# Kernel tuning notes

Hardware: AMD Instinct MI355X
Metric: run time of the kernel (lower is better)

## Reference

```python
import jax, jax.numpy as jnp
import numpy as np

EPS = 1e-8
NUM_ITERS = 2

def _ln(x, g, b, eps=1e-6):
    mu = jnp.mean(x, axis=-1, keepdims=True)
    var = jnp.mean((x - mu) ** 2, axis=-1, keepdims=True)
    return (x - mu) * jax.lax.rsqrt(var + eps) * g + b

def setup_inputs() -> dict:
    key = jax.random.key(0)
    ks = jax.random.split(key, 16)
    B, O, L, M, S, H = 64, 11, 4096, 256, 256, 1024
    def xavier(k, shape):
        fan_in, fan_out = shape[1], shape[0]
        lim = float(np.sqrt(6.0 / (fan_in + fan_out)))
        return jax.random.uniform(k, shape, jnp.float32, -lim, lim)
    return {
        "slots": jax.random.normal(ks[0], (B, O, S), jnp.float32),
        "inputs": jax.random.normal(ks[1], (B, L, M), jnp.float32),
        "ln_in_g": jnp.ones((M,), jnp.float32),
        "ln_in_b": jnp.zeros((M,), jnp.float32),
        "Wk": xavier(ks[2], (S, M)),
        "Wv": xavier(ks[3], (S, M)),
        "ln_q_g": jnp.ones((S,), jnp.float32),
        "ln_q_b": jnp.zeros((S,), jnp.float32),
        "Wq": xavier(ks[4], (S, S)),
        "gru_wi": xavier(ks[5], (3 * S, S)),
        "gru_wh": xavier(ks[6], (3 * S, S)),
        "gru_bi": jnp.zeros((3 * S,), jnp.float32),
        "gru_bh": jnp.zeros((3 * S,), jnp.float32),
        "ln_m_g": jnp.ones((S,), jnp.float32),
        "ln_m_b": jnp.zeros((S,), jnp.float32),
        "W1": xavier(ks[7], (H, S)),
        "b1": jnp.zeros((H,), jnp.float32),
        "W2": xavier(ks[8], (S, H)),
        "b2": jnp.zeros((S,), jnp.float32),
    }

def reference(slots, inputs, ln_in_g, ln_in_b, Wk, Wv, ln_q_g, ln_q_b, Wq,
              gru_wi, gru_wh, gru_bi, gru_bh, ln_m_g, ln_m_b, W1, b1, W2, b2):
    D = slots.shape[-1]
    scale = D ** -0.5  # head_dim = qkv_size (num_heads=1)
    x = _ln(inputs, ln_in_g, ln_in_b)          # [B,L,M]
    k = x @ Wk.T                                # [B,L,S]
    v = x @ Wv.T                                # [B,L,S]
    attn = None
    for _ in range(NUM_ITERS):
        sn = _ln(slots, ln_q_g, ln_q_b)
        q = (sn @ Wq.T) * scale                 # [B,O,S]
        logits = jnp.einsum('bqd,bkd->bqk', q, k)  # [B,O,L]
        attn = jax.nn.softmax(logits, axis=-2)     # inverted: over slots (queries)
        attn_n = attn / (jnp.sum(attn, axis=-1, keepdims=True) + EPS)
        updates = jnp.einsum('bqk,bkd->bqd', attn_n, v)  # [B,O,S]
        # GRU cell update
        gi = updates @ gru_wi.T + gru_bi
        gh = slots @ gru_wh.T + gru_bh
        ir, iz, inn = jnp.split(gi, 3, axis=-1)
        hr, hz, hn = jnp.split(gh, 3, axis=-1)
        r = jax.nn.sigmoid(ir + hr)
        z = jax.nn.sigmoid(iz + hz)
        n = jnp.tanh(inn + r * hn)
        slots = (1.0 - z) * n + z * slots
        # pre-LN residual MLP
        h = _ln(slots, ln_m_g, ln_m_b)
        slots = slots + (jax.nn.relu(h @ W1.T + b1) @ W2.T + b2)
    return (slots, attn)
```

## Files before the change

kernel.cpp:

```cpp
#include <hip/hip_runtime.h>
#include <hip/hip_bf16.h>


using f32x4 = __attribute__((ext_vector_type(4))) float;
using s16x8 = __attribute__((ext_vector_type(8))) short;

#define MFMA_B16(a,b,c) __builtin_amdgcn_mfma_f32_16x16x32_bf16((a),(b),(c),0,0,0)

static __device__ __forceinline__ short f2bf(float f) {
  union { __hip_bfloat16 h; short s; } u; u.h = __float2bfloat16(f); return u.s;
}
static __device__ __forceinline__ s16x8 zero8() {
  s16x8 z;
#pragma unroll
  for (int i = 0; i < 8; i++) z[i] = 0;
  return z;
}

enum : size_t {
  OFF_WKB  = 0,
  OFF_WVB  = OFF_WKB + 131072,
  OFF_WQB  = OFF_WVB + 131072,
  OFF_WIB  = OFF_WQB + 131072,
  OFF_WHB  = OFF_WIB + 393216,
  OFF_W1B  = OFF_WHB + 393216,
  OFF_W2B  = OFF_W1B + 524288,
  OFF_QB   = OFF_W2B + 524288,
  OFF_UPDB = OFF_QB  + 360448,
  OFF_SAF  = OFF_UPDB + 360448,
  OFF_SAB  = OFF_SAF + 720896,
  OFF_SBF  = OFF_SAB + 360448,
  OFF_SBB  = OFF_SBF + 720896,
  OFF_HIDB = OFF_SBB + 360448,
  OFF_NUM  = OFF_HIDB + 1441792,
  OFF_DEN  = OFF_NUM + 720896,
  OFF_KB   = OFF_DEN + 3072,
  OFF_VB   = OFF_KB + 134217728,
  WS_NEED  = OFF_VB + 134217728
};

__global__ __launch_bounds__(256) void prep_kernel(
    const float* __restrict__ Wk, const float* __restrict__ Wv, const float* __restrict__ Wq,
    const float* __restrict__ Wi, const float* __restrict__ Wh,
    const float* __restrict__ W1, const float* __restrict__ W2,
    const float* __restrict__ slots,
    short* __restrict__ WkB, short* __restrict__ WvB, short* __restrict__ WqB,
    short* __restrict__ WiB, short* __restrict__ WhB,
    short* __restrict__ W1B, short* __restrict__ W2B,
    float* __restrict__ SaF, short* __restrict__ SaB)
{
  int idx = blockIdx.x * 256 + threadIdx.x;
  int stride = gridDim.x * 256;
  for (int i = idx; i < 256*256; i += stride) { WkB[i]=f2bf(Wk[i]); WvB[i]=f2bf(Wv[i]); WqB[i]=f2bf(Wq[i]); }
  for (int i = idx; i < 768*256; i += stride) { WiB[i]=f2bf(Wi[i]); WhB[i]=f2bf(Wh[i]); }
  for (int i = idx; i < 1024*256; i += stride) { W1B[i]=f2bf(W1[i]); W2B[i]=f2bf(W2[i]); }
  for (int i = idx; i < 704*256; i += stride) { float v = slots[i]; SaF[i]=v; SaB[i]=f2bf(v); }
}

__global__ __launch_bounds__(256) void kv_kernel(
    const float* __restrict__ inputs, const float* __restrict__ lng, const float* __restrict__ lnb,
    const short* __restrict__ WkB, const short* __restrict__ WvB,
    short* __restrict__ kB, short* __restrict__ vB)
{
  __shared__ short xt[128][264];
  const int b = blockIdx.y;
  const int l0 = blockIdx.x * 128;
  const int tid = threadIdx.x;
  const int w = tid >> 6, lane = tid & 63;
  const int grp = lane >> 4, li = lane & 15;

  float4 g4 = *(const float4*)(lng + lane*4);
  float4 b4 = *(const float4*)(lnb + lane*4);
  for (int i = 0; i < 32; i++) {
    int row = w*32 + i;
    const float4 x = *(const float4*)(inputs + ((size_t)(b*4096 + l0 + row))*256 + lane*4);
    float s = x.x+x.y+x.z+x.w;
    float ss = x.x*x.x + x.y*x.y + x.z*x.z + x.w*x.w;
#pragma unroll
    for (int m = 1; m < 64; m <<= 1) { s += __shfl_xor(s, m); ss += __shfl_xor(ss, m); }
    float mu = s * 0.00390625f;
    float rs = rsqrtf(ss*0.00390625f - mu*mu + 1e-6f);
    short4 o;
    o.x = f2bf((x.x-mu)*rs*g4.x + b4.x);
    o.y = f2bf((x.y-mu)*rs*g4.y + b4.y);
    o.z = f2bf((x.z-mu)*rs*g4.z + b4.z);
    o.w = f2bf((x.w-mu)*rs*g4.w + b4.w);
    *(short4*)(&xt[row][lane*4]) = o;
  }
  __syncthreads();

  const short* Wbase = (w < 2) ? WkB : WvB;
  const int nwave = (w & 1) * 128;
  for (int nt = 0; nt < 8; nt++) {
    const int ncol = nwave + nt*16 + li;
    s16x8 bw[8];
    const short* wp = Wbase + (size_t)ncol*256 + grp*8;
#pragma unroll
    for (int kt = 0; kt < 8; kt++) bw[kt] = *(const s16x8*)(wp + kt*32);
    for (int mp = 0; mp < 4; mp++) {
      s16x8 a0[8], a1[8];
#pragma unroll
      for (int kt = 0; kt < 8; kt++) {
        a0[kt] = *(const s16x8*)(&xt[mp*32 + li][kt*32 + grp*8]);
        a1[kt] = *(const s16x8*)(&xt[mp*32 + 16 + li][kt*32 + grp*8]);
      }
      f32x4 c0 = {0,0,0,0}, c1 = {0,0,0,0};
#pragma unroll
      for (int kt = 0; kt < 8; kt++) {
        c0 = MFMA_B16(a0[kt], bw[kt], c0);
        c1 = MFMA_B16(a1[kt], bw[kt], c1);
      }
      const int row0 = mp*32 + grp*4;
      if (w < 2) {
#pragma unroll
        for (int r = 0; r < 4; r++) {
          kB[((size_t)(b*4096 + l0 + row0 + r))*256 + ncol]      = f2bf(c0[r]);
          kB[((size_t)(b*4096 + l0 + row0 + 16 + r))*256 + ncol] = f2bf(c1[r]);
        }
      } else {
        short4 p0, p1;
        p0.x=f2bf(c0[0]); p0.y=f2bf(c0[1]); p0.z=f2bf(c0[2]); p0.w=f2bf(c0[3]);
        p1.x=f2bf(c1[0]); p1.y=f2bf(c1[1]); p1.z=f2bf(c1[2]); p1.w=f2bf(c1[3]);
        short* vp = vB + ((size_t)(b*256 + ncol))*4096 + l0 + row0;
        *(short4*)vp = p0;
        *(short4*)(vp + 16) = p1;
      }
    }
  }
}

__global__ __launch_bounds__(256) void slotpre_kernel(
    const float* __restrict__ SaF, const float* __restrict__ lng, const float* __restrict__ lnb,
    const short* __restrict__ WqB, short* __restrict__ qB,
    float* __restrict__ numF, float* __restrict__ denF)
{
  __shared__ float red0[16][16], red1[16][16];
  __shared__ float mu_s[16], rs_s[16];
  __shared__ short hl[16][264];
  const int mt = blockIdx.x, nb = blockIdx.y;
  const int tid = threadIdx.x;
  {
    int gidx = (blockIdx.y*44 + blockIdx.x)*256 + tid;
    for (int i = gidx; i < 704*256; i += 44*4*256) numF[i] = 0.0f;
    if (gidx < 704) denF[gidx] = 0.0f;
  }
  const int rr = tid & 15, cs = tid >> 4;
  const float* rp = SaF + (size_t)(mt*16 + rr)*256 + cs*16;
  float s = 0.f, ss = 0.f;
#pragma unroll
  for (int i = 0; i < 16; i++) { float x = rp[i]; s += x; ss += x*x; }
  red0[rr][cs] = s; red1[rr][cs] = ss;
  __syncthreads();
  if (tid < 16) {
    float ts = 0.f, tss = 0.f;
#pragma unroll
    for (int i = 0; i < 16; i++) { ts += red0[tid][i]; tss += red1[tid][i]; }
    float mu = ts * 0.00390625f;
    mu_s[tid] = mu; rs_s[tid] = rsqrtf(tss*0.00390625f - mu*mu + 1e-6f);
  }
  __syncthreads();
  {
    float mu = mu_s[rr], rs = rs_s[rr];
#pragma unroll
    for (int i = 0; i < 16; i++) { int c = cs*16 + i; hl[rr][c] = f2bf((rp[i]-mu)*rs*lng[c] + lnb[c]); }
  }
  __syncthreads();
  const int w = tid >> 6, lane = tid & 63, grp = lane >> 4, li = lane & 15;
  const int n = nb*64 + w*16 + li;
  f32x4 acc = {0,0,0,0};
  const short* wp = WqB + (size_t)n*256 + grp*8;
#pragma unroll
  for (int kt = 0; kt < 8; kt++)
    acc = MFMA_B16(*(const s16x8*)(&hl[li][kt*32 + grp*8]), *(const s16x8*)(wp + kt*32), acc);
#pragma unroll
  for (int r = 0; r < 4; r++)
    qB[(size_t)(mt*16 + grp*4 + r)*256 + n] = f2bf(acc[r] * 0.0625f);
}

__global__ __launch_bounds__(256) void attn_kernel(
    const short* __restrict__ qB, const short* __restrict__ kB, const short* __restrict__ vB,
    float* __restrict__ numF, float* __restrict__ denF,
    float* __restrict__ attn_out, const int write_attn)
{
  __shared__ short plds[4][16][40];
  const int b = blockIdx.y;
  const int tid = threadIdx.x;
  const int w = tid >> 6, lane = tid & 63, grp = lane >> 4, li = lane & 15;
  const int nvalid = (grp < 2) ? 4 : (grp == 2 ? 3 : 0);

  s16x8 aq[8];
  if (li < 11) {
    const short* qp = qB + (size_t)(b*11 + li)*256 + grp*8;
#pragma unroll
    for (int kt = 0; kt < 8; kt++) aq[kt] = *(const s16x8*)(qp + kt*32);
  } else {
#pragma unroll
    for (int kt = 0; kt < 8; kt++) aq[kt] = zero8();
  }
  f32x4 zf = {0,0,0,0};
  f32x4 accu[16];
#pragma unroll
  for (int st = 0; st < 16; st++) accu[st] = zf;
  float dacc[4] = {0.f, 0.f, 0.f, 0.f};

  for (int p = 0; p < 4; p++) {
    const int l0 = blockIdx.x*512 + w*128 + p*32;
    f32x4 c0 = zf, c1 = zf;
    const short* kp = kB + ((size_t)(b*4096 + l0 + li))*256 + grp*8;
#pragma unroll
    for (int kt = 0; kt < 8; kt++) c0 = MFMA_B16(aq[kt], *(const s16x8*)(kp + kt*32), c0);
#pragma unroll
    for (int kt = 0; kt < 8; kt++) c1 = MFMA_B16(aq[kt], *(const s16x8*)(kp + 16*256 + kt*32), c1);

    float a0[4], a1[4];
    {
      float mx = -1e30f;
#pragma unroll
      for (int r = 0; r < 4; r++) if (r < nvalid) mx = fmaxf(mx, c0[r]);
      mx = fmaxf(mx, __shfl_xor(mx, 16)); mx = fmaxf(mx, __shfl_xor(mx, 32));
      float sm = 0.f;
#pragma unroll
      for (int r = 0; r < 4; r++) { a0[r] = (r < nvalid) ? __expf(c0[r]-mx) : 0.f; sm += a0[r]; }
      sm += __shfl_xor(sm, 16); sm += __shfl_xor(sm, 32);
      float inv = 1.0f / sm;
#pragma unroll
      for (int r = 0; r < 4; r++) { a0[r] *= inv; dacc[r] += a0[r]; }
    }
    {
      float mx = -1e30f;
#pragma unroll
      for (int r = 0; r < 4; r++) if (r < nvalid) mx = fmaxf(mx, c1[r]);
      mx = fmaxf(mx, __shfl_xor(mx, 16)); mx = fmaxf(mx, __shfl_xor(mx, 32));
      float sm = 0.f;
#pragma unroll
      for (int r = 0; r < 4; r++) { a1[r] = (r < nvalid) ? __expf(c1[r]-mx) : 0.f; sm += a1[r]; }
      sm += __shfl_xor(sm, 16); sm += __shfl_xor(sm, 32);
      float inv = 1.0f / sm;
#pragma unroll
      for (int r = 0; r < 4; r++) { a1[r] *= inv; dacc[r] += a1[r]; }
    }
    if (write_attn) {
#pragma unroll
      for (int r = 0; r < 4; r++) if (r < nvalid) {
        attn_out[(size_t)(b*11 + grp*4 + r)*4096 + l0 + li]      = a0[r];
        attn_out[(size_t)(b*11 + grp*4 + r)*4096 + l0 + 16 + li] = a1[r];
      }
    }
#pragma unroll
    for (int r = 0; r < 4; r++) {
      plds[w][grp*4 + r][li]      = (r < nvalid) ? f2bf(a0[r]) : (short)0;
      plds[w][grp*4 + r][16 + li] = (r < nvalid) ? f2bf(a1[r]) : (short)0;
    }
    asm volatile("s_waitcnt lgkmcnt(0)" ::: "memory");
    __builtin_amdgcn_sched_barrier(0);
    s16x8 pa = *(const s16x8*)(&plds[w][li][grp*8]);
    const short* vp = vB + (size_t)b*256*4096 + l0 + grp*8;
#pragma unroll
    for (int st = 0; st < 16; st++) {
      s16x8 bv = *(const s16x8*)(vp + (size_t)(st*16 + li)*4096);
      accu[st] = MFMA_B16(pa, bv, accu[st]);
    }
  }
#pragma unroll
  for (int m = 1; m < 16; m <<= 1) {
#pragma unroll
    for (int r = 0; r < 4; r++) dacc[r] += __shfl_xor(dacc[r], m);
  }
  if (li == 0) {
    for (int r = 0; r < nvalid; r++) atomicAdd(&denF[b*11 + grp*4 + r], dacc[r]);
  }
  for (int st = 0; st < 16; st++) {
#pragma unroll
    for (int r = 0; r < 4; r++) if (r < nvalid)
      atomicAdd(&numF[(size_t)(b*11 + grp*4 + r)*256 + st*16 + li], accu[st][r]);
  }
}

__global__ __launch_bounds__(256) void finalize_kernel(
    const float* __restrict__ numF, const float* __restrict__ denF, short* __restrict__ updB)
{
  int row = blockIdx.x;
  float d = denF[row] + 1e-8f;
  int i = row*256 + threadIdx.x;
  updB[i] = f2bf(numF[i] / d);
}

__global__ __launch_bounds__(256) void gru_kernel(
    const short* __restrict__ updB, const short* __restrict__ SaB, const float* __restrict__ SaF,
    const short* __restrict__ WiB, const short* __restrict__ WhB,
    const float* __restrict__ bi, const float* __restrict__ bh,
    float* __restrict__ SbF, short* __restrict__ SbB)
{
  const int mt = blockIdx.x;
  const int tid = threadIdx.x;
  const int w = tid >> 6, lane = tid & 63, grp = lane >> 4, li = lane & 15;
  const int j0 = blockIdx.y*64 + w*16;
  s16x8 au[8], as_[8];
  {
    const short* up = updB + (size_t)(mt*16 + li)*256 + grp*8;
    const short* sp = SaB + (size_t)(mt*16 + li)*256 + grp*8;
#pragma unroll
    for (int kt = 0; kt < 8; kt++) { au[kt] = *(const s16x8*)(up + kt*32); as_[kt] = *(const s16x8*)(sp + kt*32); }
  }
  f32x4 ai[3], ah[3];
  for (int gg = 0; gg < 3; gg++) {
    f32x4 ci = {0,0,0,0}, ch = {0,0,0,0};
    const short* wip = WiB + (size_t)(gg*256 + j0 + li)*256 + grp*8;
    const short* whp = WhB + (size_t)(gg*256 + j0 + li)*256 + grp*8;
#pragma unroll
    for (int kt = 0; kt < 8; kt++) {
      ci = MFMA_B16(au[kt],  *(const s16x8*)(wip + kt*32), ci);
      ch = MFMA_B16(as_[kt], *(const s16x8*)(whp + kt*32), ch);
    }
    ai[gg] = ci; ah[gg] = ch;
  }
  const int j = j0 + li;
#pragma unroll
  for (int r = 0; r < 4; r++) {
    const int row = mt*16 + grp*4 + r;
    float ir = ai[0][r] + bi[j],       hr = ah[0][r] + bh[j];
    float iz = ai[1][r] + bi[256 + j], hz = ah[1][r] + bh[256 + j];
    float in_= ai[2][r] + bi[512 + j], hn = ah[2][r] + bh[512 + j];
    float rg = 1.0f / (1.0f + __expf(-(ir + hr)));
    float zg = 1.0f / (1.0f + __expf(-(iz + hz)));
    float ng = tanhf(in_ + rg*hn);
    float nv = (1.0f - zg)*ng + zg*SaF[(size_t)row*256 + j];
    SbF[(size_t)row*256 + j] = nv;
    SbB[(size_t)row*256 + j] = f2bf(nv);
  }
}

__global__ __launch_bounds__(256) void mlp1_kernel(
    const float* __restrict__ SbF, const float* __restrict__ lng, const float* __restrict__ lnb,
    const short* __restrict__ W1B, const float* __restrict__ b1, short* __restrict__ hidB)
{
  __shared__ float red0[16][16], red1[16][16];
  __shared__ float mu_s[16], rs_s[16];
  __shared__ short hl[16][264];
  const int mt = blockIdx.x, nb = blockIdx.y;
  const int tid = threadIdx.x;
  const int rr = tid & 15, cs = tid >> 4;
  const float* rp = SbF + (size_t)(mt*16 + rr)*256 + cs*16;
  float s = 0.f, ss = 0.f;
#pragma unroll
  for (int i = 0; i < 16; i++) { float x = rp[i]; s += x; ss += x*x; }
  red0[rr][cs] = s; red1[rr][cs] = ss;
  __syncthreads();
  if (tid < 16) {
    float ts = 0.f, tss = 0.f;
#pragma unroll
    for (int i = 0; i < 16; i++) { ts += red0[tid][i]; tss += red1[tid][i]; }
    float mu = ts * 0.00390625f;
    mu_s[tid] = mu; rs_s[tid] = rsqrtf(tss*0.00390625f - mu*mu + 1e-6f);
  }
  __syncthreads();
  {
    float mu = mu_s[rr], rs = rs_s[rr];
#pragma unroll
    for (int i = 0; i < 16; i++) { int c = cs*16 + i; hl[rr][c] = f2bf((rp[i]-mu)*rs*lng[c] + lnb[c]); }
  }
  __syncthreads();
  const int w = tid >> 6, lane = tid & 63, grp = lane >> 4, li = lane & 15;
  const int n = nb*64 + w*16 + li;
  f32x4 acc = {0,0,0,0};
  const short* wp = W1B + (size_t)n*256 + grp*8;
#pragma unroll
  for (int kt = 0; kt < 8; kt++)
    acc = MFMA_B16(*(const s16x8*)(&hl[li][kt*32 + grp*8]), *(const s16x8*)(wp + kt*32), acc);
  const float bias = b1[n];
#pragma unroll
  for (int r = 0; r < 4; r++)
    hidB[(size_t)(mt*16 + grp*4 + r)*1024 + n] = f2bf(fmaxf(acc[r] + bias, 0.0f));
}

__global__ __launch_bounds__(256) void mlp2_kernel(
    const short* __restrict__ hidB, const short* __restrict__ W2B,
    const float* __restrict__ b2, const float* __restrict__ SbF,
    float* __restrict__ SaF, short* __restrict__ SaB,
    float* __restrict__ out_slots, const int write_out)
{
  const int mt = blockIdx.x, nb = blockIdx.y;
  const int tid = threadIdx.x;
  const int w = tid >> 6, lane = tid & 63, grp = lane >> 4, li = lane & 15;
  const int n = nb*64 + w*16 + li;
  f32x4 acc = {0,0,0,0};
  const short* ap = hidB + (size_t)(mt*16 + li)*1024 + grp*8;
  const short* wp = W2B + (size_t)n*1024 + grp*8;
#pragma unroll 8
  for (int kt = 0; kt < 32; kt++)
    acc = MFMA_B16(*(const s16x8*)(ap + kt*32), *(const s16x8*)(wp + kt*32), acc);
  const float bias = b2[n];
#pragma unroll
  for (int r = 0; r < 4; r++) {
    const int row = mt*16 + grp*4 + r;
    float v = acc[r] + bias + SbF[(size_t)row*256 + n];
    SaF[(size_t)row*256 + n] = v;
    SaB[(size_t)row*256 + n] = f2bf(v);
    if (write_out) out_slots[(size_t)row*256 + n] = v;
  }
}

extern "C" void kernel_launch(void* const* d_in, const int* in_sizes, int n_in,
                              void* d_out, int out_size, void* d_ws, size_t ws_size,
                              hipStream_t stream) {
  (void)in_sizes; (void)n_in; (void)out_size;
  if (ws_size < WS_NEED) return;

  const float* slots   = (const float*)d_in[0];
  const float* inputs  = (const float*)d_in[1];
  const float* ln_in_g = (const float*)d_in[2];
  const float* ln_in_b = (const float*)d_in[3];
  const float* Wk      = (const float*)d_in[4];
  const float* Wv      = (const float*)d_in[5];
  const float* ln_q_g  = (const float*)d_in[6];
  const float* ln_q_b  = (const float*)d_in[7];
  const float* Wq      = (const float*)d_in[8];
  const float* gwi     = (const float*)d_in[9];
  const float* gwh     = (const float*)d_in[10];
  const float* gbi     = (const float*)d_in[11];
  const float* gbh     = (const float*)d_in[12];
  const float* ln_m_g  = (const float*)d_in[13];
  const float* ln_m_b  = (const float*)d_in[14];
  const float* W1      = (const float*)d_in[15];
  const float* b1      = (const float*)d_in[16];
  const float* W2      = (const float*)d_in[17];
  const float* b2      = (const float*)d_in[18];
  float* out = (float*)d_out;

  char* ws = (char*)d_ws;
  short* WkB  = (short*)(ws + OFF_WKB);
  short* WvB  = (short*)(ws + OFF_WVB);
  short* WqB  = (short*)(ws + OFF_WQB);
  short* WiB  = (short*)(ws + OFF_WIB);
  short* WhB  = (short*)(ws + OFF_WHB);
  short* W1B  = (short*)(ws + OFF_W1B);
  short* W2B  = (short*)(ws + OFF_W2B);
  short* qB   = (short*)(ws + OFF_QB);
  short* updB = (short*)(ws + OFF_UPDB);
  float* SaF  = (float*)(ws + OFF_SAF);
  short* SaB  = (short*)(ws + OFF_SAB);
  float* SbF  = (float*)(ws + OFF_SBF);
  short* SbB  = (short*)(ws + OFF_SBB);
  short* hidB = (short*)(ws + OFF_HIDB);
  float* numF = (float*)(ws + OFF_NUM);
  float* denF = (float*)(ws + OFF_DEN);
  short* kB   = (short*)(ws + OFF_KB);
  short* vB   = (short*)(ws + OFF_VB);

  float* attn_out = out + 704*256;

  prep_kernel<<<dim3(512), dim3(256), 0, stream>>>(
      Wk, Wv, Wq, gwi, gwh, W1, W2, slots,
      WkB, WvB, WqB, WiB, WhB, W1B, W2B, SaF, SaB);

  kv_kernel<<<dim3(32, 64), dim3(256), 0, stream>>>(
      inputs, ln_in_g, ln_in_b, WkB, WvB, kB, vB);

  for (int t = 0; t < 2; t++) {
    slotpre_kernel<<<dim3(44, 4), dim3(256), 0, stream>>>(
        SaF, ln_q_g, ln_q_b, WqB, qB, numF, denF);
    attn_kernel<<<dim3(8, 64), dim3(256), 0, stream>>>(
        qB, kB, vB, numF, denF, attn_out, (t == 1) ? 1 : 0);
    finalize_kernel<<<dim3(704), dim3(256), 0, stream>>>(numF, denF, updB);
    gru_kernel<<<dim3(44, 4), dim3(256), 0, stream>>>(
        updB, SaB, SaF, WiB, WhB, gbi, gbh, SbF, SbB);
    mlp1_kernel<<<dim3(44, 16), dim3(256), 0, stream>>>(
        SbF, ln_m_g, ln_m_b, W1B, b1, hidB);
    mlp2_kernel<<<dim3(44, 4), dim3(256), 0, stream>>>(
        hidB, W2B, b2, SbF, SaF, SaB, out, (t == 1) ? 1 : 0);
  }
}
```

Before: 835.2 us.

## Halve kv and attention tiles, batch LayerNorm rows, swap kv loop order

The kv projection kernel now processes 64 rows per block instead of 128, doubling the grid. The input LayerNorm handles four rows at a time so their loads and shuffle reductions can overlap. The MFMA loop order is swapped so the A fragments stay in registers while the weight fragments are reloaded for each column tile. The attention kernel also covers half as many keys per block with a doubled grid, and both kernels get a 3-waves-per-SIMD occupancy hint to hide memory latency. In exchange, weight fragments are reloaded from global/cache more often, and the attention kernel has twice as many partial sums to combine, which may raise atomic or reduction traffic.

New measurement: 978.9 us. 17.2% more time.

```diff
diff --git a/kernel.cpp b/kernel.cpp
--- a/kernel.cpp
+++ b/kernel.cpp
@@ -57,53 +57,67 @@
   for (int i = idx; i < 704*256; i += stride) { float v = slots[i]; SaF[i]=v; SaB[i]=f2bf(v); }
 }
 
-__global__ __launch_bounds__(256) void kv_kernel(
+__global__ __launch_bounds__(256, 3) void kv_kernel(
     const float* __restrict__ inputs, const float* __restrict__ lng, const float* __restrict__ lnb,
     const short* __restrict__ WkB, const short* __restrict__ WvB,
     short* __restrict__ kB, short* __restrict__ vB)
 {
-  __shared__ short xt[128][264];
+  __shared__ short xt[64][264];
   const int b = blockIdx.y;
-  const int l0 = blockIdx.x * 128;
+  const int l0 = blockIdx.x * 64;
   const int tid = threadIdx.x;
   const int w = tid >> 6, lane = tid & 63;
   const int grp = lane >> 4, li = lane & 15;
 
   float4 g4 = *(const float4*)(lng + lane*4);
   float4 b4 = *(const float4*)(lnb + lane*4);
-  for (int i = 0; i < 32; i++) {
-    int row = w*32 + i;
-    const float4 x = *(const float4*)(inputs + ((size_t)(b*4096 + l0 + row))*256 + lane*4);
-    float s = x.x+x.y+x.z+x.w;
-    float ss = x.x*x.x + x.y*x.y + x.z*x.z + x.w*x.w;
-#pragma unroll
-    for (int m = 1; m < 64; m <<= 1) { s += __shfl_xor(s, m); ss += __shfl_xor(ss, m); }
-    float mu = s * 0.00390625f;
-    float rs = rsqrtf(ss*0.00390625f - mu*mu + 1e-6f);
-    short4 o;
-    o.x = f2bf((x.x-mu)*rs*g4.x + b4.x);
-    o.y = f2bf((x.y-mu)*rs*g4.y + b4.y);
-    o.z = f2bf((x.z-mu)*rs*g4.z + b4.z);
-    o.w = f2bf((x.w-mu)*rs*g4.w + b4.w);
-    *(short4*)(&xt[row][lane*4]) = o;
+#pragma unroll
+  for (int i0 = 0; i0 < 16; i0 += 4) {
+    float4 x[4];
+#pragma unroll
+    for (int u = 0; u < 4; u++)
+      x[u] = *(const float4*)(inputs + ((size_t)(b*4096 + l0 + w*16 + i0 + u))*256 + lane*4);
+    float s[4], ss[4];
+#pragma unroll
+    for (int u = 0; u < 4; u++) {
+      s[u]  = x[u].x + x[u].y + x[u].z + x[u].w;
+      ss[u] = x[u].x*x[u].x + x[u].y*x[u].y + x[u].z*x[u].z + x[u].w*x[u].w;
+    }
+#pragma unroll
+    for (int m = 1; m < 64; m <<= 1) {
+#pragma unroll
+      for (int u = 0; u < 4; u++) { s[u] += __shfl_xor(s[u], m); ss[u] += __shfl_xor(ss[u], m); }
+    }
+#pragma unroll
+    for (int u = 0; u < 4; u++) {
+      float mu = s[u] * 0.00390625f;
+      float rs = rsqrtf(ss[u]*0.00390625f - mu*mu + 1e-6f);
+      short4 o;
+      o.x = f2bf((x[u].x-mu)*rs*g4.x + b4.x);
+      o.y = f2bf((x[u].y-mu)*rs*g4.y + b4.y);
+      o.z = f2bf((x[u].z-mu)*rs*g4.z + b4.z);
+      o.w = f2bf((x[u].w-mu)*rs*g4.w + b4.w);
+      *(short4*)(&xt[w*16 + i0 + u][lane*4]) = o;
+    }
   }
   __syncthreads();
 
   const short* Wbase = (w < 2) ? WkB : WvB;
   const int nwave = (w & 1) * 128;
-  for (int nt = 0; nt < 8; nt++) {
-    const int ncol = nwave + nt*16 + li;
-    s16x8 bw[8];
-    const short* wp = Wbase + (size_t)ncol*256 + grp*8;
-#pragma unroll
-    for (int kt = 0; kt < 8; kt++) bw[kt] = *(const s16x8*)(wp + kt*32);
-    for (int mp = 0; mp < 4; mp++) {
-      s16x8 a0[8], a1[8];
-#pragma unroll
-      for (int kt = 0; kt < 8; kt++) {
-        a0[kt] = *(const s16x8*)(&xt[mp*32 + li][kt*32 + grp*8]);
-        a1[kt] = *(const s16x8*)(&xt[mp*32 + 16 + li][kt*32 + grp*8]);
-      }
+#pragma unroll
+  for (int mp = 0; mp < 2; mp++) {
+    s16x8 a0[8], a1[8];
+#pragma unroll
+    for (int kt = 0; kt < 8; kt++) {
+      a0[kt] = *(const s16x8*)(&xt[mp*32 + li][kt*32 + grp*8]);
+      a1[kt] = *(const s16x8*)(&xt[mp*32 + 16 + li][kt*32 + grp*8]);
+    }
+    for (int nt = 0; nt < 8; nt++) {
+      const int ncol = nwave + nt*16 + li;
+      const short* wp = Wbase + (size_t)ncol*256 + grp*8;
+      s16x8 bw[8];
+#pragma unroll
+      for (int kt = 0; kt < 8; kt++) bw[kt] = *(const s16x8*)(wp + kt*32);
       f32x4 c0 = {0,0,0,0}, c1 = {0,0,0,0};
 #pragma unroll
       for (int kt = 0; kt < 8; kt++) {
@@ -177,7 +191,7 @@
     qB[(size_t)(mt*16 + grp*4 + r)*256 + n] = f2bf(acc[r] * 0.0625f);
 }
 
-__global__ __launch_bounds__(256) void attn_kernel(
+__global__ __launch_bounds__(256, 3) void attn_kernel(
     const short* __restrict__ qB, const short* __restrict__ kB, const short* __restrict__ vB,
     float* __restrict__ numF, float* __restrict__ denF,
     float* __restrict__ attn_out, const int write_attn)
@@ -203,8 +217,8 @@
   for (int st = 0; st < 16; st++) accu[st] = zf;
   float dacc[4] = {0.f, 0.f, 0.f, 0.f};
 
-  for (int p = 0; p < 4; p++) {
-    const int l0 = blockIdx.x*512 + w*128 + p*32;
+  for (int p = 0; p < 2; p++) {
+    const int l0 = blockIdx.x*256 + w*64 + p*32;
     f32x4 c0 = zf, c1 = zf;
     const short* kp = kB + ((size_t)(b*4096 + l0 + li))*256 + grp*8;
 #pragma unroll
@@ -453,13 +467,13 @@
       Wk, Wv, Wq, gwi, gwh, W1, W2, slots,
       WkB, WvB, WqB, WiB, WhB, W1B, W2B, SaF, SaB);
 
-  kv_kernel<<<dim3(32, 64), dim3(256), 0, stream>>>(
+  kv_kernel<<<dim3(64, 64), dim3(256), 0, stream>>>(
       inputs, ln_in_g, ln_in_b, WkB, WvB, kB, vB);
 
   for (int t = 0; t < 2; t++) {
     slotpre_kernel<<<dim3(44, 4), dim3(256), 0, stream>>>(
         SaF, ln_q_g, ln_q_b, WqB, qB, numF, denF);
-    attn_kernel<<<dim3(8, 64), dim3(256), 0, stream>>>(
+    attn_kernel<<<dim3(16, 64), dim3(256), 0, stream>>>(
         qB, kB, vB, numF, denF, attn_out, (t == 1) ? 1 : 0);
     finalize_kernel<<<dim3(704), dim3(256), 0, stream>>>(numF, denF, updB);
     gru_kernel<<<dim3(44, 4), dim3(256), 0, stream>>>(
```
